# Optimization experiments

Hardware: AMD Instinct MI355X
Metric: run time of the kernel (lower is better)

## Reference

```python
import jax, jax.numpy as jnp
import numpy as np

EPS = 1e-8

def l2norm(x, axis):
    # matches torch: x / (sqrt(sum(x^2)) + eps)
    return x / (jnp.sqrt(jnp.sum(x * x, axis=axis, keepdims=True)) + EPS)

def setup_inputs() -> dict:
    key = jax.random.key(0)
    kq, kc, kwq, kbq, kwk, kbk = jax.random.split(key, 6)
    B, QL, SL, D = 128, 512, 1024, 1024
    query = jax.random.normal(kq, (B, QL, D), dtype=jnp.float32)
    context = jax.random.normal(kc, (B, SL, D), dtype=jnp.float32)
    s = 1.0 / np.sqrt(D)
    Wq = jax.random.uniform(kwq, (D, D), jnp.float32, -s, s)
    bq = jax.random.uniform(kbq, (D,), jnp.float32, -s, s)
    Wk = jax.random.uniform(kwk, (D, D), jnp.float32, -s, s)
    bk = jax.random.uniform(kbk, (D,), jnp.float32, -s, s)
    return {"query": query, "context": context, "Wq": Wq, "bq": bq,
            "Wk": Wk, "bk": bk, "smooth": 9.0}

def reference(query, context, Wq, bq, Wk, bk, smooth):
    # linear projections (nn.Linear: x @ W^T + b)
    sim_k = jnp.einsum('bsd,ed->bse', context, Wk) + bk   # (B, SL, D)
    sim_q = jnp.einsum('bqd,ed->bqe', query, Wq) + bq     # (B, QL, D)
    # scores: bmm(sim_k, sim_q^T) -> (B, SL, QL)
    attn = jnp.einsum('bse,bqe->bsq', sim_k, sim_q)
    attn = jnp.where(attn >= 0, attn, 0.1 * attn)          # LeakyReLU(0.1)
    attn = l2norm(attn, axis=2)                            # over queryL dim
    # transpose -> (B, QL, SL), scale, softmax over sourceL
    attn = jax.nn.softmax(attn.transpose(0, 2, 1) * smooth, axis=2)
    # weighted sum of raw context (sim_v = context; fcv unused in original)
    wc = jnp.einsum('bqs,bsd->bqd', attn, context)         # (B, QL, D)
    return l2norm(wc, axis=-1)
```

## Files before the change

kernel.cpp:

```cpp
#include <hip/hip_runtime.h>
#include <hip/hip_bf16.h>

typedef __attribute__((ext_vector_type(8))) short bf16x8;
typedef __attribute__((ext_vector_type(4))) float f32x4;
typedef __attribute__((ext_vector_type(4))) unsigned short u16x4;
typedef __attribute__((ext_vector_type(8))) unsigned short u16x8;

#define DEVINL static __device__ __forceinline__

DEVINL unsigned short f2bf(float f) {
  union { float f; unsigned u; } a; a.f = f;
  return (unsigned short)((a.u + 0x7fffu + ((a.u >> 16) & 1u)) >> 16);
}
DEVINL float bf2f(unsigned short s) {
  union { unsigned u; float f; } a; a.u = ((unsigned)s) << 16; return a.f;
}

typedef __attribute__((address_space(1))) const unsigned char ga_u8;
typedef __attribute__((address_space(3))) unsigned char ls_u8;

constexpr int KD = 1024;
constexpr int NKT = KD / 64;


#define STAGE(b_, mat_, kt_) do { \
    const unsigned short* src_ = (mat_) == 0 ? Az : Bz; \
    const int br_ = (mat_) == 0 ? m0 : n0; \
    char* dst_ = lds + (b_) * 65536 + (mat_) * 32768; \
    _Pragma("unroll") \
    for (int i_ = 0; i_ < 4; ++i_) { \
      const unsigned short* g_ = src_ + (size_t)(br_ + i_ * 64 + sr) * KD + (kt_) * 64 + gc * 8; \
      __builtin_amdgcn_global_load_lds((ga_u8*)g_, (ls_u8*)(dst_ + (i_ * 512 + wv * 64) * 16), 16, 0, 0); \
    } \
  } while (0)

#define KSUB(b_, ks_, STG) do { \
    const char* pA_ = lds + (b_) * 65536; \
    const char* pB_ = pA_ + 32768; \
    const int co_ = (((ks_) * 4 + kg) ^ (ml & 7)) << 4; \
    bf16x8 af_[8], bf_[4]; \
    _Pragma("unroll") \
    for (int mi = 0; mi < 8; ++mi) \
      af_[mi] = *(const bf16x8*)(pA_ + (wm * 128 + mi * 16 + ml) * 128 + co_); \
    _Pragma("unroll") \
    for (int ni = 0; ni < 4; ++ni) \
      bf_[ni] = *(const bf16x8*)(pB_ + (wn * 64 + ni * 16 + ml) * 128 + co_); \
    STG; \
    __builtin_amdgcn_s_setprio(1); \
    _Pragma("unroll") \
    for (int mi = 0; mi < 8; ++mi) \
    _Pragma("unroll") \
    for (int ni = 0; ni < 4; ++ni) \
      acc[mi][ni] = __builtin_amdgcn_mfma_f32_16x16x32_bf16(af_[mi], bf_[ni], acc[mi][ni], 0, 0, 0); \
    __builtin_amdgcn_s_setprio(0); \
  } while (0)

template<int MODE>
__global__ __launch_bounds__(512, 2) void gemm8(
    const unsigned short* __restrict__ A, const unsigned short* __restrict__ B,
    const float* __restrict__ bias, void* __restrict__ Cv,
    float* __restrict__ rnorm2, int mtiles,
    long long sAz, long long sBz, long long sCz, long long sRz, long long sBiasz)
{
  alignas(16) __shared__ char lds[131072];

  const int tid = threadIdx.x;
  const int lane = tid & 63;
  const int wv = tid >> 6;
  const int wm = wv >> 2;
  const int wn = wv & 3;
  const int kg = lane >> 4;
  const int ml = lane & 15;

  const int nwg = (int)gridDim.x;
  const int bid = (int)blockIdx.x;
  const int w = (bid & 7) * (nwg >> 3) + (bid >> 3);
  const int bpz = mtiles * 4;
  const int z = w / bpz;
  const int rem = w - z * bpz;
  const int mt = rem >> 2, nt = rem & 3;
  const int m0 = mt * 256, n0 = nt * 256;

  const unsigned short* Az = A + (size_t)z * (size_t)sAz;
  const unsigned short* Bz = B + (size_t)z * (size_t)sBz;

  const int sr = tid >> 3;
  const int gc = (tid & 7) ^ (sr & 7);

  f32x4 acc[8][4];
  const f32x4 zero4 = {0.f, 0.f, 0.f, 0.f};
#pragma unroll
  for (int i = 0; i < 8; ++i)
#pragma unroll
    for (int j = 0; j < 4; ++j) acc[i][j] = zero4;

  STAGE(0, 0, 0);
  STAGE(0, 1, 0);
  asm volatile("s_waitcnt vmcnt(0)" ::: "memory");
  __builtin_amdgcn_s_barrier();

  for (int t = 0; t < NKT; ++t) {
    const int cur = t & 1;
    const int nxt = cur ^ 1;
    if (t + 1 < NKT) {
      KSUB(cur, 0, STAGE(nxt, 0, t + 1));
      KSUB(cur, 1, STAGE(nxt, 1, t + 1));
    } else {
      KSUB(cur, 0, );
      KSUB(cur, 1, );
    }
    asm volatile("s_waitcnt vmcnt(0)" ::: "memory");
    __builtin_amdgcn_s_barrier();
  }

  float* ew = (float*)(lds + wv * 4352);
  const int erow = lane >> 3;
  const int ec8 = (lane & 7) * 8;
  const int ncol0 = n0 + wn * 64;

  if (MODE == 1) {
    const float* cb = bias + (size_t)z * (size_t)sBiasz;
    f32x4 cb4[8];
#pragma unroll
    for (int mi = 0; mi < 8; ++mi)
      cb4[mi] = *(const f32x4*)(cb + m0 + wm * 128 + mi * 16 + kg * 4);
    float* rn = rnorm2 + (size_t)z * (size_t)sRz;
#pragma unroll
    for (int ni = 0; ni < 4; ++ni) {
      float cs = 0.f;
#pragma unroll
      for (int mi = 0; mi < 8; ++mi)
#pragma unroll
        for (int j = 0; j < 4; ++j) {
          float v = acc[mi][ni][j] + cb4[mi][j];
          v = v >= 0.f ? v : 0.1f * v;
          acc[mi][ni][j] = v;
          cs += v * v;
        }
      cs += __shfl_xor(cs, 16);
      cs += __shfl_xor(cs, 32);
      if (kg == 0) atomicAdd(&rn[ncol0 + ni * 16 + ml], cs);
    }
  }

  f32x4 bv0 = zero4, bv1 = zero4;
  if (MODE == 0) {
    bv0 = *(const f32x4*)(bias + ncol0 + ec8);
    bv1 = *(const f32x4*)(bias + ncol0 + ec8 + 4);
  }

#pragma unroll
  for (int mi = 0; mi < 8; ++mi) {
#pragma unroll
    for (int ni = 0; ni < 4; ++ni)
#pragma unroll
      for (int j = 0; j < 4; ++j)
        ew[(kg * 4 + j) * 68 + ni * 16 + ml] = acc[mi][ni][j];
    const int rb = m0 + wm * 128 + mi * 16;
#pragma unroll
    for (int i = 0; i < 2; ++i) {
      const int r = erow + 8 * i;
      f32x4 x = *(const f32x4*)(&ew[r * 68 + ec8]);
      f32x4 y = *(const f32x4*)(&ew[r * 68 + ec8 + 4]);
      if (MODE == 0 || MODE == 3) {
        unsigned short* C = (unsigned short*)Cv + (size_t)z * (size_t)sCz;
        union { unsigned short s[8]; u16x8 v; } u;
        u.s[0]=f2bf(x[0]+bv0[0]); u.s[1]=f2bf(x[1]+bv0[1]);
        u.s[2]=f2bf(x[2]+bv0[2]); u.s[3]=f2bf(x[3]+bv0[3]);
        u.s[4]=f2bf(y[0]+bv1[0]); u.s[5]=f2bf(y[1]+bv1[1]);
        u.s[6]=f2bf(y[2]+bv1[2]); u.s[7]=f2bf(y[3]+bv1[3]);
        *(u16x8*)(C + (size_t)(rb + r) * 1024 + ncol0 + ec8) = u.v;
      } else {
        float* C = (float*)Cv + (size_t)z * (size_t)sCz;
        *(f32x4*)(C + (size_t)(rb + r) * 1024 + ncol0 + ec8) = x;
        *(f32x4*)(C + (size_t)(rb + r) * 1024 + ncol0 + ec8 + 4) = y;
      }
    }
  }
}

__global__ __launch_bounds__(256) void cvt_bf16_k(
    const float* __restrict__ src, unsigned short* __restrict__ dst)
{
  size_t i = ((size_t)blockIdx.x * 256 + threadIdx.x) * 8;
  f32x4 x = *(const f32x4*)(src + i);
  f32x4 y = *(const f32x4*)(src + i + 4);
  union { unsigned short s[8]; u16x8 v; } u;
  u.s[0]=f2bf(x[0]); u.s[1]=f2bf(x[1]); u.s[2]=f2bf(x[2]); u.s[3]=f2bf(x[3]);
  u.s[4]=f2bf(y[0]); u.s[5]=f2bf(y[1]); u.s[6]=f2bf(y[2]); u.s[7]=f2bf(y[3]);
  *(u16x8*)(dst + i) = u.v;
}

__global__ __launch_bounds__(256) void wT_k(
    const float* __restrict__ W, unsigned short* __restrict__ WT)
{
  __shared__ float tile[32][36];
  const int t = threadIdx.x;
  const int e0 = blockIdx.x * 32, d0 = blockIdx.y * 32;
  const int r = t >> 3, c4 = (t & 7) * 4;
  f32x4 v = *(const f32x4*)(W + (size_t)(e0 + r) * 1024 + d0 + c4);
  *(f32x4*)(&tile[r][c4]) = v;
  __syncthreads();
  u16x4 o;
  o[0] = f2bf(tile[c4 + 0][r]); o[1] = f2bf(tile[c4 + 1][r]);
  o[2] = f2bf(tile[c4 + 2][r]); o[3] = f2bf(tile[c4 + 3][r]);
  *(u16x4*)(WT + (size_t)(d0 + r) * 1024 + e0 + c4) = o;
}

__global__ __launch_bounds__(256) void convert_ctx_k(
    const float* __restrict__ src, unsigned short* __restrict__ dstT,
    unsigned short* __restrict__ dstR)
{
  __shared__ float tile[32][36];
  const int t = threadIdx.x;
  const int s0 = blockIdx.x * 32, d0 = blockIdx.y * 32;
  const float* S = src + (size_t)blockIdx.z * 1048576;
  unsigned short* DT = dstT + (size_t)blockIdx.z * 1048576;
  unsigned short* DR = dstR + (size_t)blockIdx.z * 1048576;
  const int s = t >> 3, d4 = (t & 7) * 4;
  f32x4 v = *(const f32x4*)(S + (size_t)(s0 + s) * 1024 + d0 + d4);
  u16x4 r;
  r[0] = f2bf(v[0]); r[1] = f2bf(v[1]); r[2] = f2bf(v[2]); r[3] = f2bf(v[3]);
  *(u16x4*)(DR + (size_t)(s0 + s) * 1024 + d0 + d4) = r;
  *(f32x4*)(&tile[s][d4]) = v;
  __syncthreads();
  const int d = t >> 3, s4 = (t & 7) * 4;
  u16x4 o;
  o[0] = f2bf(tile[s4 + 0][d]); o[1] = f2bf(tile[s4 + 1][d]);
  o[2] = f2bf(tile[s4 + 2][d]); o[3] = f2bf(tile[s4 + 3][d]);
  *(u16x4*)(DT + (size_t)(d0 + d) * 1024 + s0 + s4) = o;
}

__global__ __launch_bounds__(256) void cdot_k(
    const unsigned short* __restrict__ simq, const float* __restrict__ bk,
    float* __restrict__ cq)
{
  __shared__ float shs[4];
  const int t = threadIdx.x;
  const unsigned short* row = simq + (size_t)blockIdx.x * 1024;
  u16x4 a = *(const u16x4*)(row + t * 4);
  f32x4 b = *(const f32x4*)(bk + t * 4);
  float d = bf2f(a[0]) * b[0] + bf2f(a[1]) * b[1] +
            bf2f(a[2]) * b[2] + bf2f(a[3]) * b[3];
#pragma unroll
  for (int o = 32; o; o >>= 1) d += __shfl_xor(d, o);
  if ((t & 63) == 0) shs[t >> 6] = d;
  __syncthreads();
  if (t == 0) cq[blockIdx.x] = shs[0] + shs[1] + shs[2] + shs[3];
}

__global__ __launch_bounds__(256) void softmax_k(
    const float* __restrict__ S, const float* __restrict__ rnorm2,
    const float* __restrict__ smoothp, unsigned short* __restrict__ P)
{
  __shared__ float shm[4], shs[4];
  const int t = threadIdx.x;
  const int z = blockIdx.x >> 9;
  const float sm = *smoothp;
  f32x4 s4 = ((const f32x4*)(S + (size_t)blockIdx.x * 1024))[t];
  f32x4 r4 = ((const f32x4*)(rnorm2 + (size_t)z * 1024))[t];
  f32x4 lg;
  lg[0] = sm * s4[0] / (sqrtf(r4[0]) + 1e-8f);
  lg[1] = sm * s4[1] / (sqrtf(r4[1]) + 1e-8f);
  lg[2] = sm * s4[2] / (sqrtf(r4[2]) + 1e-8f);
  lg[3] = sm * s4[3] / (sqrtf(r4[3]) + 1e-8f);
  float mx = fmaxf(fmaxf(lg[0], lg[1]), fmaxf(lg[2], lg[3]));
#pragma unroll
  for (int o = 32; o; o >>= 1) mx = fmaxf(mx, __shfl_xor(mx, o));
  if ((t & 63) == 0) shm[t >> 6] = mx;
  __syncthreads();
  mx = fmaxf(fmaxf(shm[0], shm[1]), fmaxf(shm[2], shm[3]));
  f32x4 e;
  e[0] = __expf(lg[0] - mx); e[1] = __expf(lg[1] - mx);
  e[2] = __expf(lg[2] - mx); e[3] = __expf(lg[3] - mx);
  float sum = e[0] + e[1] + e[2] + e[3];
#pragma unroll
  for (int o = 32; o; o >>= 1) sum += __shfl_xor(sum, o);
  if ((t & 63) == 0) shs[t >> 6] = sum;
  __syncthreads();
  sum = shs[0] + shs[1] + shs[2] + shs[3];
  float inv = 1.f / sum;
  u16x4 p;
  p[0] = f2bf(e[0] * inv); p[1] = f2bf(e[1] * inv);
  p[2] = f2bf(e[2] * inv); p[3] = f2bf(e[3] * inv);
  ((u16x4*)(P + (size_t)blockIdx.x * 1024))[t] = p;
}

__global__ __launch_bounds__(256) void l2norm_k(
    const float* __restrict__ W, float* __restrict__ O)
{
  __shared__ float shs[4];
  const int t = threadIdx.x;
  f32x4 v = ((const f32x4*)(W + (size_t)blockIdx.x * 1024))[t];
  float ss = v[0]*v[0] + v[1]*v[1] + v[2]*v[2] + v[3]*v[3];
#pragma unroll
  for (int o = 32; o; o >>= 1) ss += __shfl_xor(ss, o);
  if ((t & 63) == 0) shs[t >> 6] = ss;
  __syncthreads();
  ss = shs[0] + shs[1] + shs[2] + shs[3];
  float inv = 1.f / (sqrtf(ss) + 1e-8f);
  f32x4 o4 = { v[0]*inv, v[1]*inv, v[2]*inv, v[3]*inv };
  ((f32x4*)(O + (size_t)blockIdx.x * 1024))[t] = o4;
}

extern "C" void kernel_launch(void* const* d_in, const int* in_sizes, int n_in,
                              void* d_out, int out_size, void* d_ws, size_t ws_size,
                              hipStream_t stream)
{
  (void)in_sizes; (void)n_in; (void)out_size;
  const float* query   = (const float*)d_in[0];
  const float* context = (const float*)d_in[1];
  const float* Wq = (const float*)d_in[2];
  const float* bq = (const float*)d_in[3];
  const float* Wk = (const float*)d_in[4];
  const float* bk = (const float*)d_in[5];
  const float* smooth = (const float*)d_in[6];
  float* out = (float*)d_out;

  const int B = 128, QL = 512, SL = 1024, D = 1024;

  const size_t perB =
      (size_t)QL * D * 2 + (size_t)SL * D * 2 + (size_t)D * SL * 2 +
      (size_t)QL * D * 2 + (size_t)QL * D * 2 + (size_t)QL * SL * 4 +
      (size_t)SL * 4 + (size_t)QL * 4 + 4096;
  const size_t fixed = 2 * (size_t)D * D * 2 + 8192;
  size_t usable = ws_size > fixed ? ws_size - fixed : 0;
  int C = (int)(usable / perB);
  if (C > B) C = B;
  if (C < 1) C = 1;

  char* p = (char*)d_ws;
  auto alloc = [&](size_t bytes) {
    char* r = p; p += (bytes + 255) & ~(size_t)255; return r;
  };
  unsigned short* wqbf = (unsigned short*)alloc((size_t)D * D * 2);
  unsigned short* wkT  = (unsigned short*)alloc((size_t)D * D * 2);
  unsigned short* qbf  = (unsigned short*)alloc((size_t)C * QL * D * 2);
  unsigned short* ctxbf= (unsigned short*)alloc((size_t)C * SL * D * 2);
  unsigned short* ctxT = (unsigned short*)alloc((size_t)C * D * SL * 2);
  unsigned short* simq = (unsigned short*)alloc((size_t)C * QL * D * 2);
  unsigned short* ubf  = (unsigned short*)alloc((size_t)C * QL * D * 2);
  float* Sbuf = (float*)alloc((size_t)C * QL * SL * 4);
  float* rn   = (float*)alloc((size_t)C * SL * 4);
  float* cq   = (float*)alloc((size_t)C * QL * 4);

  cvt_bf16_k<<<dim3(D * D / 2048), 256, 0, stream>>>(Wq, wqbf);
  wT_k<<<dim3(32, 32), 256, 0, stream>>>(Wk, wkT);

  for (int b0 = 0; b0 < B; b0 += C) {
    const int Cc = (B - b0) < C ? (B - b0) : C;
    hipMemsetAsync(rn, 0, (size_t)Cc * SL * 4, stream);
    cvt_bf16_k<<<dim3(Cc * QL * D / 2048), 256, 0, stream>>>(
        query + (size_t)b0 * QL * D, qbf);
    convert_ctx_k<<<dim3(32, 32, Cc), 256, 0, stream>>>(
        context + (size_t)b0 * SL * D, ctxT, ctxbf);
    gemm8<0><<<dim3(Cc * 8), 512, 0, stream>>>(
        qbf, wqbf, bq, simq, nullptr, 2,
        (long long)QL * D, 0, (long long)QL * D, 0, 0);
    gemm8<3><<<dim3(Cc * 8), 512, 0, stream>>>(
        simq, wkT, nullptr, ubf, nullptr, 2,
        (long long)QL * D, 0, (long long)QL * D, 0, 0);
    cdot_k<<<dim3(Cc * QL), 256, 0, stream>>>(simq, bk, cq);
    gemm8<1><<<dim3(Cc * 8), 512, 0, stream>>>(
        ubf, ctxbf, cq, Sbuf, rn, 2,
        (long long)QL * D, (long long)SL * D, (long long)QL * SL,
        (long long)SL, (long long)QL);
    softmax_k<<<Cc * QL, 256, 0, stream>>>(Sbuf, rn, smooth, simq );
    gemm8<2><<<dim3(Cc * 8), 512, 0, stream>>>(
        simq , ctxT, nullptr, Sbuf , nullptr, 2,
        (long long)QL * SL, (long long)D * SL, (long long)QL * D, 0, 0);
    l2norm_k<<<Cc * QL, 256, 0, stream>>>(Sbuf, out + (size_t)b0 * QL * D);
  }
}
```

Baseline: 1.141 ms.

## Shrink GEMM tile to 256x128 with triple-buffered 32-wide K pipeline

Reworks the batched bf16 GEMM kernel to use 256x128 output tiles with a 4x2 wave layout and per-wave 64x64 accumulators. K is staged in 32-element slices through a three-deep LDS ring with partial vmcnt waits, replacing the 64-element double buffer. LDS drops to 72KB and launch bounds ask for 4 blocks per CU, so more workgroups run at once and memory latency is better hidden. The trade-off is smaller tiles with less data reuse, more barriers per K step, and a doubled grid. The epilogue indexing is adjusted to match.

```diff
diff --git a/kernel.cpp b/kernel.cpp
--- a/kernel.cpp
+++ b/kernel.cpp
@@ -20,98 +20,101 @@
 typedef __attribute__((address_space(3))) unsigned char ls_u8;
 
 constexpr int KD = 1024;
-constexpr int NKT = KD / 64;
-
-
-#define STAGE(b_, mat_, kt_) do { \
-    const unsigned short* src_ = (mat_) == 0 ? Az : Bz; \
-    const int br_ = (mat_) == 0 ? m0 : n0; \
-    char* dst_ = lds + (b_) * 65536 + (mat_) * 32768; \
+
+
+#define VM3 asm volatile("s_waitcnt vmcnt(3)" ::: "memory")
+#define VM0 asm volatile("s_waitcnt vmcnt(0)" ::: "memory")
+
+#define STAGE3(buf_) do { \
+    char* d_ = lds + (buf_) * 24576 + wv * 1024; \
+    __builtin_amdgcn_global_load_lds((ga_u8*)gA0, (ls_u8*)d_, 16, 0, 0); \
+    __builtin_amdgcn_global_load_lds((ga_u8*)gA1, (ls_u8*)(d_ + 8192), 16, 0, 0); \
+    __builtin_amdgcn_global_load_lds((ga_u8*)gB0, (ls_u8*)(d_ + 16384), 16, 0, 0); \
+    gA0 += 32; gA1 += 32; gB0 += 32; \
+  } while (0)
+
+#define TILE3(rb_, STG, WT_, BR_) do { \
+    const char* pA_ = lds + (rb_) * 24576; \
+    const char* pB_ = pA_ + 16384; \
+    bf16x8 af_[4], bf_[4]; \
+    STG; \
     _Pragma("unroll") \
-    for (int i_ = 0; i_ < 4; ++i_) { \
-      const unsigned short* g_ = src_ + (size_t)(br_ + i_ * 64 + sr) * KD + (kt_) * 64 + gc * 8; \
-      __builtin_amdgcn_global_load_lds((ga_u8*)g_, (ls_u8*)(dst_ + (i_ * 512 + wv * 64) * 16), 16, 0, 0); \
-    } \
-  } while (0)
-
-#define KSUB(b_, ks_, STG) do { \
-    const char* pA_ = lds + (b_) * 65536; \
-    const char* pB_ = pA_ + 32768; \
-    const int co_ = (((ks_) * 4 + kg) ^ (ml & 7)) << 4; \
-    bf16x8 af_[8], bf_[4]; \
-    _Pragma("unroll") \
-    for (int mi = 0; mi < 8; ++mi) \
-      af_[mi] = *(const bf16x8*)(pA_ + (wm * 128 + mi * 16 + ml) * 128 + co_); \
+    for (int mi = 0; mi < 4; ++mi) \
+      af_[mi] = *(const bf16x8*)(pA_ + offA + mi * 1024); \
     _Pragma("unroll") \
     for (int ni = 0; ni < 4; ++ni) \
-      bf_[ni] = *(const bf16x8*)(pB_ + (wn * 64 + ni * 16 + ml) * 128 + co_); \
-    STG; \
+      bf_[ni] = *(const bf16x8*)(pB_ + offB + ni * 1024); \
     __builtin_amdgcn_s_setprio(1); \
     _Pragma("unroll") \
-    for (int mi = 0; mi < 8; ++mi) \
+    for (int mi = 0; mi < 4; ++mi) \
     _Pragma("unroll") \
     for (int ni = 0; ni < 4; ++ni) \
       acc[mi][ni] = __builtin_amdgcn_mfma_f32_16x16x32_bf16(af_[mi], bf_[ni], acc[mi][ni], 0, 0, 0); \
     __builtin_amdgcn_s_setprio(0); \
+    WT_; \
+    BR_; \
   } while (0)
 
+#define BARR __builtin_amdgcn_s_barrier()
+
 template<int MODE>
-__global__ __launch_bounds__(512, 2) void gemm8(
+__global__ __launch_bounds__(512, 4) void gemm8(
     const unsigned short* __restrict__ A, const unsigned short* __restrict__ B,
     const float* __restrict__ bias, void* __restrict__ Cv,
     float* __restrict__ rnorm2, int mtiles,
     long long sAz, long long sBz, long long sCz, long long sRz, long long sBiasz)
 {
-  alignas(16) __shared__ char lds[131072];
+  alignas(16) __shared__ char lds[73728];
 
   const int tid = threadIdx.x;
   const int lane = tid & 63;
   const int wv = tid >> 6;
-  const int wm = wv >> 2;
-  const int wn = wv & 3;
+  const int wm = wv >> 1;
+  const int wn = wv & 1;
   const int kg = lane >> 4;
   const int ml = lane & 15;
 
   const int nwg = (int)gridDim.x;
   const int bid = (int)blockIdx.x;
   const int w = (bid & 7) * (nwg >> 3) + (bid >> 3);
-  const int bpz = mtiles * 4;
+  const int bpz = mtiles * 8;
   const int z = w / bpz;
   const int rem = w - z * bpz;
-  const int mt = rem >> 2, nt = rem & 3;
-  const int m0 = mt * 256, n0 = nt * 256;
+  const int mt = rem >> 3, nt = rem & 7;
+  const int m0 = mt * 256, n0 = nt * 128;
 
   const unsigned short* Az = A + (size_t)z * (size_t)sAz;
   const unsigned short* Bz = B + (size_t)z * (size_t)sBz;
 
   const int sr = tid >> 3;
-  const int gc = (tid & 7) ^ (sr & 7);
-
-  f32x4 acc[8][4];
+  const int un = (tid & 7) ^ (sr & 7);
+  const int hi = un >> 2, kc = un & 3;
+  const unsigned short* gA0 = Az + (size_t)(m0 + sr * 2 + hi) * KD + kc * 8;
+  const unsigned short* gA1 = Az + (size_t)(m0 + 128 + sr * 2 + hi) * KD + kc * 8;
+  const unsigned short* gB0 = Bz + (size_t)(n0 + sr * 2 + hi) * KD + kc * 8;
+
+  const int swz = (((ml & 1) << 2) + kg) ^ ((ml >> 1) & 7);
+  const int offA = (wm * 32 + (ml >> 1)) * 128 + swz * 16;
+  const int offB = (wn * 32 + (ml >> 1)) * 128 + swz * 16;
+
+  f32x4 acc[4][4];
   const f32x4 zero4 = {0.f, 0.f, 0.f, 0.f};
 #pragma unroll
-  for (int i = 0; i < 8; ++i)
+  for (int i = 0; i < 4; ++i)
 #pragma unroll
     for (int j = 0; j < 4; ++j) acc[i][j] = zero4;
 
-  STAGE(0, 0, 0);
-  STAGE(0, 1, 0);
-  asm volatile("s_waitcnt vmcnt(0)" ::: "memory");
-  __builtin_amdgcn_s_barrier();
-
-  for (int t = 0; t < NKT; ++t) {
-    const int cur = t & 1;
-    const int nxt = cur ^ 1;
-    if (t + 1 < NKT) {
-      KSUB(cur, 0, STAGE(nxt, 0, t + 1));
-      KSUB(cur, 1, STAGE(nxt, 1, t + 1));
-    } else {
-      KSUB(cur, 0, );
-      KSUB(cur, 1, );
-    }
-    asm volatile("s_waitcnt vmcnt(0)" ::: "memory");
-    __builtin_amdgcn_s_barrier();
-  }
+  STAGE3(0); STAGE3(1);
+  VM3; BARR;
+
+  for (int tt = 0; tt < 30; tt += 3) {
+    TILE3(0, STAGE3(2), VM3, BARR);
+    TILE3(1, STAGE3(0), VM3, BARR);
+    TILE3(2, STAGE3(1), VM3, BARR);
+  }
+  TILE3(0, (void)0, VM0, BARR);
+  TILE3(1, (void)0, (void)0, (void)0);
+  __syncthreads();
 
   float* ew = (float*)(lds + wv * 4352);
   const int erow = lane >> 3;
@@ -120,16 +123,16 @@
 
   if (MODE == 1) {
     const float* cb = bias + (size_t)z * (size_t)sBiasz;
-    f32x4 cb4[8];
-#pragma unroll
-    for (int mi = 0; mi < 8; ++mi)
-      cb4[mi] = *(const f32x4*)(cb + m0 + wm * 128 + mi * 16 + kg * 4);
+    f32x4 cb4[4];
+#pragma unroll
+    for (int mi = 0; mi < 4; ++mi)
+      cb4[mi] = *(const f32x4*)(cb + m0 + wm * 64 + mi * 16 + kg * 4);
     float* rn = rnorm2 + (size_t)z * (size_t)sRz;
 #pragma unroll
     for (int ni = 0; ni < 4; ++ni) {
       float cs = 0.f;
 #pragma unroll
-      for (int mi = 0; mi < 8; ++mi)
+      for (int mi = 0; mi < 4; ++mi)
 #pragma unroll
         for (int j = 0; j < 4; ++j) {
           float v = acc[mi][ni][j] + cb4[mi][j];
@@ -150,13 +153,13 @@
   }
 
 #pragma unroll
-  for (int mi = 0; mi < 8; ++mi) {
+  for (int mi = 0; mi < 4; ++mi) {
 #pragma unroll
     for (int ni = 0; ni < 4; ++ni)
 #pragma unroll
       for (int j = 0; j < 4; ++j)
         ew[(kg * 4 + j) * 68 + ni * 16 + ml] = acc[mi][ni][j];
-    const int rb = m0 + wm * 128 + mi * 16;
+    const int rb = m0 + wm * 64 + mi * 16;
 #pragma unroll
     for (int i = 0; i < 2; ++i) {
       const int r = erow + 8 * i;
@@ -354,19 +357,19 @@
         query + (size_t)b0 * QL * D, qbf);
     convert_ctx_k<<<dim3(32, 32, Cc), 256, 0, stream>>>(
         context + (size_t)b0 * SL * D, ctxT, ctxbf);
-    gemm8<0><<<dim3(Cc * 8), 512, 0, stream>>>(
+    gemm8<0><<<dim3(Cc * 16), 512, 0, stream>>>(
         qbf, wqbf, bq, simq, nullptr, 2,
         (long long)QL * D, 0, (long long)QL * D, 0, 0);
-    gemm8<3><<<dim3(Cc * 8), 512, 0, stream>>>(
+    gemm8<3><<<dim3(Cc * 16), 512, 0, stream>>>(
         simq, wkT, nullptr, ubf, nullptr, 2,
         (long long)QL * D, 0, (long long)QL * D, 0, 0);
     cdot_k<<<dim3(Cc * QL), 256, 0, stream>>>(simq, bk, cq);
-    gemm8<1><<<dim3(Cc * 8), 512, 0, stream>>>(
+    gemm8<1><<<dim3(Cc * 16), 512, 0, stream>>>(
         ubf, ctxbf, cq, Sbuf, rn, 2,
         (long long)QL * D, (long long)SL * D, (long long)QL * SL,
         (long long)SL, (long long)QL);
     softmax_k<<<Cc * QL, 256, 0, stream>>>(Sbuf, rn, smooth, simq );
-    gemm8<2><<<dim3(Cc * 8), 512, 0, stream>>>(
+    gemm8<2><<<dim3(Cc * 16), 512, 0, stream>>>(
         simq , ctxT, nullptr, Sbuf , nullptr, 2,
         (long long)QL * SL, (long long)D * SL, (long long)QL * D, 0, 0);
     l2norm_k<<<Cc * QL, 256, 0, stream>>>(Sbuf, out + (size_t)b0 * QL * D);
```

Result: slower. 1.240 ms (+8.7%).

## Fold query and key projections into one precomputed weight product

Applied to the files above, without the earlier changes.

Precomputes Wu = Wq^T·Wk plus the folded bias vectors once, so the query-side path needs a single GEMM per batch instead of two GEMMs. The bias cross term for the score offset is computed from the raw query against a precomputed vector. This removes one large per-batch GEMM and the intermediate simq buffer, freeing workspace for larger batch chunks. The cost is a one-time DxD GEMM and extra bf16 rounding of the fused weight, which changes numerical error.

```diff
diff --git a/kernel.cpp b/kernel.cpp
--- a/kernel.cpp
+++ b/kernel.cpp
@@ -231,17 +231,39 @@
   *(u16x4*)(DT + (size_t)(d0 + d) * 1024 + s0 + s4) = o;
 }
 
-__global__ __launch_bounds__(256) void cdot_k(
-    const unsigned short* __restrict__ simq, const float* __restrict__ bk,
-    float* __restrict__ cq)
+__global__ __launch_bounds__(256) void rowdot_k(
+    const unsigned short* __restrict__ Mbf, const float* __restrict__ vec,
+    float* __restrict__ outv)
 {
   __shared__ float shs[4];
   const int t = threadIdx.x;
-  const unsigned short* row = simq + (size_t)blockIdx.x * 1024;
+  const unsigned short* row = Mbf + (size_t)blockIdx.x * 1024;
   u16x4 a = *(const u16x4*)(row + t * 4);
-  f32x4 b = *(const f32x4*)(bk + t * 4);
+  f32x4 b = *(const f32x4*)(vec + t * 4);
   float d = bf2f(a[0]) * b[0] + bf2f(a[1]) * b[1] +
             bf2f(a[2]) * b[2] + bf2f(a[3]) * b[3];
+#pragma unroll
+  for (int o = 32; o; o >>= 1) d += __shfl_xor(d, o);
+  if ((t & 63) == 0) shs[t >> 6] = d;
+  __syncthreads();
+  if (t == 0) outv[blockIdx.x] = shs[0] + shs[1] + shs[2] + shs[3];
+}
+
+__global__ __launch_bounds__(256) void cdot_k(
+    const unsigned short* __restrict__ qbf, const float* __restrict__ vb,
+    const float* __restrict__ bq, const float* __restrict__ bk,
+    float* __restrict__ cq)
+{
+  __shared__ float shs[4];
+  const int t = threadIdx.x;
+  const unsigned short* row = qbf + (size_t)blockIdx.x * 1024;
+  u16x4 a = *(const u16x4*)(row + t * 4);
+  f32x4 b = *(const f32x4*)(vb + t * 4);
+  f32x4 p = *(const f32x4*)(bq + t * 4);
+  f32x4 k = *(const f32x4*)(bk + t * 4);
+  float d = bf2f(a[0]) * b[0] + bf2f(a[1]) * b[1] +
+            bf2f(a[2]) * b[2] + bf2f(a[3]) * b[3] +
+            p[0] * k[0] + p[1] * k[1] + p[2] * k[2] + p[3] * k[3];
 #pragma unroll
   for (int o = 32; o; o >>= 1) d += __shfl_xor(d, o);
   if ((t & 63) == 0) shs[t >> 6] = d;
@@ -321,9 +343,9 @@
 
   const size_t perB =
       (size_t)QL * D * 2 + (size_t)SL * D * 2 + (size_t)D * SL * 2 +
-      (size_t)QL * D * 2 + (size_t)QL * D * 2 + (size_t)QL * SL * 4 +
+      (size_t)QL * D * 2 + (size_t)QL * SL * 4 +
       (size_t)SL * 4 + (size_t)QL * 4 + 4096;
-  const size_t fixed = 2 * (size_t)D * D * 2 + 8192;
+  const size_t fixed = 3 * (size_t)D * D * 2 + 2 * (size_t)D * 4 + 16384;
   size_t usable = ws_size > fixed ? ws_size - fixed : 0;
   int C = (int)(usable / perB);
   if (C > B) C = B;
@@ -333,19 +355,25 @@
   auto alloc = [&](size_t bytes) {
     char* r = p; p += (bytes + 255) & ~(size_t)255; return r;
   };
-  unsigned short* wqbf = (unsigned short*)alloc((size_t)D * D * 2);
+  unsigned short* wqT  = (unsigned short*)alloc((size_t)D * D * 2);
   unsigned short* wkT  = (unsigned short*)alloc((size_t)D * D * 2);
+  unsigned short* WuT  = (unsigned short*)alloc((size_t)D * D * 2);
+  float* cu = (float*)alloc((size_t)D * 4);
+  float* vb = (float*)alloc((size_t)D * 4);
   unsigned short* qbf  = (unsigned short*)alloc((size_t)C * QL * D * 2);
   unsigned short* ctxbf= (unsigned short*)alloc((size_t)C * SL * D * 2);
   unsigned short* ctxT = (unsigned short*)alloc((size_t)C * D * SL * 2);
-  unsigned short* simq = (unsigned short*)alloc((size_t)C * QL * D * 2);
   unsigned short* ubf  = (unsigned short*)alloc((size_t)C * QL * D * 2);
   float* Sbuf = (float*)alloc((size_t)C * QL * SL * 4);
   float* rn   = (float*)alloc((size_t)C * SL * 4);
   float* cq   = (float*)alloc((size_t)C * QL * 4);
 
-  cvt_bf16_k<<<dim3(D * D / 2048), 256, 0, stream>>>(Wq, wqbf);
+  wT_k<<<dim3(32, 32), 256, 0, stream>>>(Wq, wqT);
   wT_k<<<dim3(32, 32), 256, 0, stream>>>(Wk, wkT);
+  rowdot_k<<<dim3(D), 256, 0, stream>>>(wkT, bq, cu);
+  rowdot_k<<<dim3(D), 256, 0, stream>>>(wqT, bk, vb);
+  gemm8<3><<<dim3(16), 512, 0, stream>>>(
+      wkT, wqT, nullptr, WuT, nullptr, 4, 0, 0, 0, 0, 0);
 
   for (int b0 = 0; b0 < B; b0 += C) {
     const int Cc = (B - b0) < C ? (B - b0) : C;
@@ -355,19 +383,16 @@
     convert_ctx_k<<<dim3(32, 32, Cc), 256, 0, stream>>>(
         context + (size_t)b0 * SL * D, ctxT, ctxbf);
     gemm8<0><<<dim3(Cc * 8), 512, 0, stream>>>(
-        qbf, wqbf, bq, simq, nullptr, 2,
+        qbf, WuT, cu, ubf, nullptr, 2,
         (long long)QL * D, 0, (long long)QL * D, 0, 0);
-    gemm8<3><<<dim3(Cc * 8), 512, 0, stream>>>(
-        simq, wkT, nullptr, ubf, nullptr, 2,
-        (long long)QL * D, 0, (long long)QL * D, 0, 0);
-    cdot_k<<<dim3(Cc * QL), 256, 0, stream>>>(simq, bk, cq);
+    cdot_k<<<dim3(Cc * QL), 256, 0, stream>>>(qbf, vb, bq, bk, cq);
     gemm8<1><<<dim3(Cc * 8), 512, 0, stream>>>(
         ubf, ctxbf, cq, Sbuf, rn, 2,
         (long long)QL * D, (long long)SL * D, (long long)QL * SL,
         (long long)SL, (long long)QL);
-    softmax_k<<<Cc * QL, 256, 0, stream>>>(Sbuf, rn, smooth, simq );
+    softmax_k<<<Cc * QL, 256, 0, stream>>>(Sbuf, rn, smooth, ubf );
     gemm8<2><<<dim3(Cc * 8), 512, 0, stream>>>(
-        simq , ctxT, nullptr, Sbuf , nullptr, 2,
+        ubf , ctxT, nullptr, Sbuf , nullptr, 2,
         (long long)QL * SL, (long long)D * SL, (long long)QL * D, 0, 0);
     l2norm_k<<<Cc * QL, 256, 0, stream>>>(Sbuf, out + (size_t)b0 * QL * D);
   }
```

After: 1.045 ms. 1.09x faster.
